# Performance work log

Hardware: AMD Instinct MI355X
Metric: run time of the kernel (lower is better)

Reference implementation:

```python
import jax, jax.numpy as jnp
import numpy as np

N, C, S = 64, 128, 12          # batch, channels, input_size
HW = S * S                      # 144
RIN = S ** 4


def setup_inputs() -> dict:
    key = jax.random.key(0)
    ks = jax.random.split(key, 6)
    x1 = jax.random.normal(ks[0], (N, C, S, S), dtype=jnp.float32)
    x2 = jax.random.normal(ks[1], (N, C, S, S), dtype=jnp.float32)
    # Linear weights stored [in, out]; scaled ~1/sqrt(fan_in) like torch default
    w1 = jax.random.normal(ks[2], (RIN, RIN // 4), dtype=jnp.float32) / np.sqrt(RIN)
    w2 = jax.random.normal(ks[3], (RIN // 4, RIN // 16), dtype=jnp.float32) / np.sqrt(RIN // 4)
    w3 = jax.random.normal(ks[4], (RIN // 16, RIN // 64), dtype=jnp.float32) / np.sqrt(RIN // 16)
    w4 = jax.random.normal(ks[5], (RIN // 64, 8), dtype=jnp.float32) / np.sqrt(RIN // 64)
    return {
        "x1": x1, "x2": x2,
        "w1": w1, "b1": jnp.zeros((RIN // 4,), jnp.float32),
        "w2": w2, "b2": jnp.zeros((RIN // 16,), jnp.float32),
        "w3": w3, "b3": jnp.zeros((RIN // 64,), jnp.float32),
        "w4": w4, "b4": jnp.zeros((8,), jnp.float32),
    }


def _l2_normalize(x):
    # torch: norm over dim=1 (channels), broadcast divide -> per-(n,h,w) unit vectors
    return x / jnp.linalg.norm(x, axis=1, keepdims=True)


def reference(x1, x2, w1, b1, w2, b2, w3, b3, w4, b4):
    n, c, h, w = x1.shape
    x1n = _l2_normalize(x1)
    x2n = _l2_normalize(x2)
    # out[n, k, i, j] = sum_c x1n[n,c,i,j] * x2n_flat[n,c,k]  (k flattens x2's HxW)
    corr = jnp.einsum('ncij,nck->nkij', x1n, x2n.reshape(n, c, h * w))  # [N, HW, H, W]
    x = corr.reshape(n, h * w * h * w)  # [N, S^4]
    x = jax.nn.relu(x @ w1 + b1)
    x = jax.nn.relu(x @ w2 + b2)
    x = jnp.tanh(x @ w3 + b3)
    H = x @ w4 + b4  # [N, 8]
    ones = jnp.ones((n, 1), dtype=H.dtype)
    return jnp.concatenate([H, ones], axis=1).reshape(n, 3, 3)
```

## Files before the change

### kernel.cpp

```cpp
#include <hip/hip_runtime.h>
#include <stdint.h>
#include <math.h>


typedef short short8 __attribute__((ext_vector_type(8)));
typedef float f32x4 __attribute__((ext_vector_type(4)));

__device__ __forceinline__ unsigned bf16u(float x) {
    return (__float_as_uint(x) + 0x8000u) >> 16;
}
__device__ __forceinline__ unsigned packbf(float a, float b) {
    return ((__float_as_uint(a) + 0x8000u) >> 16) |
           ((__float_as_uint(b) + 0x8000u) & 0xFFFF0000u);
}
__device__ __forceinline__ float bf2f(unsigned short u) {
    return __uint_as_float(((unsigned)u) << 16);
}

__global__ __launch_bounds__(1024) void kcorr2(const float* __restrict__ x1,
                                               const float* __restrict__ x2,
                                               unsigned short* __restrict__ Abuf) {
    __shared__ unsigned short s1[144 * 136];
    __shared__ unsigned short s2p[48 * 136];
    __shared__ float rn1[144], rn2p[48];
    int b = blockIdx.x;
    int n = b / 3, p = b - n * 3;
    int t = threadIdx.x;
    const float* p1 = x1 + n * 18432;
    const float* p2 = x2 + n * 18432;
#pragma unroll
    for (int i = 0; i < 18; ++i) {
        int g = t + 1024 * i;
        int c = g / 144, ij = g - c * 144;
        s1[ij * 136 + c] = (unsigned short)bf16u(p1[g]);
    }
#pragma unroll
    for (int i = 0; i < 6; ++i) {
        int g = t + 1024 * i;
        int c = g / 48, ijl = g - c * 48;
        s2p[ijl * 136 + c] = (unsigned short)bf16u(p2[c * 144 + p * 48 + ijl]);
    }
    __syncthreads();
    if (t < 144) {
        float acc = 0.f;
        for (int c = 0; c < 128; ++c) { float v = bf2f(s1[t * 136 + c]); acc += v * v; }
        rn1[t] = 1.0f / sqrtf(acc);
    } else if (t < 192) {
        int ijl = t - 144;
        float acc = 0.f;
        for (int c = 0; c < 128; ++c) { float v = bf2f(s2p[ijl * 136 + c]); acc += v * v; }
        rn2p[ijl] = 1.0f / sqrtf(acc);
    }
    __syncthreads();
    int lane = t & 63, w = t >> 6;
    int col = lane & 15, quad = lane >> 4;
    unsigned short* out = Abuf + n * 20736 + p * 48 * 144;
    for (int tt = w; tt < 27; tt += 16) {
        int ml0 = (tt / 9) * 16, n0 = (tt % 9) * 16;
        f32x4 acc = {0.f, 0.f, 0.f, 0.f};
        const short8* a0 = (const short8*)(s2p + (ml0 + col) * 136 + quad * 8);
        const short8* b0 = (const short8*)(s1 + (n0 + col) * 136 + quad * 8);
#pragma unroll
        for (int ks = 0; ks < 4; ++ks) {
            short8 a = a0[ks * 4];
            short8 bv = b0[ks * 4];
            acc = __builtin_amdgcn_mfma_f32_16x16x32_bf16(a, bv, acc, 0, 0, 0);
        }
        float rc = rn1[n0 + col];
#pragma unroll
        for (int r = 0; r < 4; ++r) {
            int rl = ml0 + quad * 4 + r;
            out[rl * 144 + n0 + col] = (unsigned short)bf16u(acc[r] * rn2p[rl] * rc);
        }
    }
}

template <int N, int KTOT, int KCHUNK>
__global__ __launch_bounds__(256) void kgemm(const unsigned short* __restrict__ A,
                                             const float* __restrict__ W,
                                             float* __restrict__ Cf) {
    int lane = threadIdx.x & 63;
    int w = threadIdx.x >> 6;
    int col = lane & 15, quad = lane >> 4;
    int c0 = blockIdx.x * 64 + w * 16;
    int kc = blockIdx.y * KCHUNK;
    const unsigned short* Ap = A + kc + quad * 8;
    const float* Wp = W + (size_t)(kc + quad * 8) * N + c0 + col;
    f32x4 acc0 = {0, 0, 0, 0}, acc1 = {0, 0, 0, 0}, acc2 = {0, 0, 0, 0}, acc3 = {0, 0, 0, 0};
#pragma unroll 2
    for (int ks = 0; ks < KCHUNK / 32; ++ks) {
        int kk = ks * 32;
        short8 a0 = *(const short8*)(Ap + (0 * 16 + col) * KTOT + kk);
        short8 a1 = *(const short8*)(Ap + (1 * 16 + col) * KTOT + kk);
        short8 a2 = *(const short8*)(Ap + (2 * 16 + col) * KTOT + kk);
        short8 a3 = *(const short8*)(Ap + (3 * 16 + col) * KTOT + kk);
        const float* wp = Wp + (size_t)kk * N;
        float b0 = wp[0 * (size_t)N];
        float b1 = wp[1 * (size_t)N];
        float b2 = wp[2 * (size_t)N];
        float b3 = wp[3 * (size_t)N];
        float b4 = wp[4 * (size_t)N];
        float b5 = wp[5 * (size_t)N];
        float b6 = wp[6 * (size_t)N];
        float b7 = wp[7 * (size_t)N];
        union { unsigned u[4]; short8 s; } bu;
        bu.u[0] = packbf(b0, b1);
        bu.u[1] = packbf(b2, b3);
        bu.u[2] = packbf(b4, b5);
        bu.u[3] = packbf(b6, b7);
        acc0 = __builtin_amdgcn_mfma_f32_16x16x32_bf16(a0, bu.s, acc0, 0, 0, 0);
        acc1 = __builtin_amdgcn_mfma_f32_16x16x32_bf16(a1, bu.s, acc1, 0, 0, 0);
        acc2 = __builtin_amdgcn_mfma_f32_16x16x32_bf16(a2, bu.s, acc2, 0, 0, 0);
        acc3 = __builtin_amdgcn_mfma_f32_16x16x32_bf16(a3, bu.s, acc3, 0, 0, 0);
    }
#pragma unroll
    for (int r = 0; r < 4; ++r) {
        int row0 = quad * 4 + r;
        atomicAdd(&Cf[(0 * 16 + row0) * N + c0 + col], acc0[r]);
        atomicAdd(&Cf[(1 * 16 + row0) * N + c0 + col], acc1[r]);
        atomicAdd(&Cf[(2 * 16 + row0) * N + c0 + col], acc2[r]);
        atomicAdd(&Cf[(3 * 16 + row0) * N + c0 + col], acc3[r]);
    }
}

template <int N, int KTOT, int KCHUNK>
__global__ __launch_bounds__(256) void kgemm2f(const float* __restrict__ Af,
                                               const float* __restrict__ bias,
                                               const float* __restrict__ W,
                                               float* __restrict__ Cf) {
    int lane = threadIdx.x & 63;
    int w = threadIdx.x >> 6;
    int col = lane & 15, quad = lane >> 4;
    int c0 = blockIdx.x * 64 + w * 16;
    if (c0 >= N) return;
    int kc = blockIdx.y * KCHUNK;
    int kb = kc + quad * 8;
    const float* Ap = Af + kb;
    const float* Wp = W + (size_t)kb * N + c0 + col;
    f32x4 acc0 = {0, 0, 0, 0}, acc1 = {0, 0, 0, 0}, acc2 = {0, 0, 0, 0}, acc3 = {0, 0, 0, 0};
#pragma unroll 2
    for (int ks = 0; ks < KCHUNK / 32; ++ks) {
        int kk = ks * 32;
        f32x4 bb0 = *(const f32x4*)(bias + kb + kk);
        f32x4 bb1 = *(const f32x4*)(bias + kb + kk + 4);
        union { unsigned u[4]; short8 s; } au[4];
#pragma unroll
        for (int i = 0; i < 4; ++i) {
            const float* ap = Ap + (size_t)(i * 16 + col) * KTOT + kk;
            f32x4 v0 = *(const f32x4*)(ap);
            f32x4 v1 = *(const f32x4*)(ap + 4);
            float r0 = fmaxf(v0[0] + bb0[0], 0.f), r1 = fmaxf(v0[1] + bb0[1], 0.f);
            float r2 = fmaxf(v0[2] + bb0[2], 0.f), r3 = fmaxf(v0[3] + bb0[3], 0.f);
            float r4 = fmaxf(v1[0] + bb1[0], 0.f), r5 = fmaxf(v1[1] + bb1[1], 0.f);
            float r6 = fmaxf(v1[2] + bb1[2], 0.f), r7 = fmaxf(v1[3] + bb1[3], 0.f);
            au[i].u[0] = packbf(r0, r1); au[i].u[1] = packbf(r2, r3);
            au[i].u[2] = packbf(r4, r5); au[i].u[3] = packbf(r6, r7);
        }
        const float* wp = Wp + (size_t)kk * N;
        float b0 = wp[0 * (size_t)N];
        float b1 = wp[1 * (size_t)N];
        float b2 = wp[2 * (size_t)N];
        float b3 = wp[3 * (size_t)N];
        float b4 = wp[4 * (size_t)N];
        float b5 = wp[5 * (size_t)N];
        float b6 = wp[6 * (size_t)N];
        float b7 = wp[7 * (size_t)N];
        union { unsigned u[4]; short8 s; } bu;
        bu.u[0] = packbf(b0, b1);
        bu.u[1] = packbf(b2, b3);
        bu.u[2] = packbf(b4, b5);
        bu.u[3] = packbf(b6, b7);
        acc0 = __builtin_amdgcn_mfma_f32_16x16x32_bf16(au[0].s, bu.s, acc0, 0, 0, 0);
        acc1 = __builtin_amdgcn_mfma_f32_16x16x32_bf16(au[1].s, bu.s, acc1, 0, 0, 0);
        acc2 = __builtin_amdgcn_mfma_f32_16x16x32_bf16(au[2].s, bu.s, acc2, 0, 0, 0);
        acc3 = __builtin_amdgcn_mfma_f32_16x16x32_bf16(au[3].s, bu.s, acc3, 0, 0, 0);
    }
#pragma unroll
    for (int r = 0; r < 4; ++r) {
        int row0 = quad * 4 + r;
        atomicAdd(&Cf[(0 * 16 + row0) * N + c0 + col], acc0[r]);
        atomicAdd(&Cf[(1 * 16 + row0) * N + c0 + col], acc1[r]);
        atomicAdd(&Cf[(2 * 16 + row0) * N + c0 + col], acc2[r]);
        atomicAdd(&Cf[(3 * 16 + row0) * N + c0 + col], acc3[r]);
    }
}

__global__ __launch_bounds__(384) void kgemm3(const float* __restrict__ C2f,
                                              const float* __restrict__ b2,
                                              const float* __restrict__ W3,
                                              float* __restrict__ C3f) {
    __shared__ float as[162];
    int n = blockIdx.x, sl = blockIdx.y;
    int t = threadIdx.x;
    int base = sl * 162;
    if (t < 162) as[t] = fmaxf(C2f[n * 1296 + base + t] + b2[base + t], 0.f);
    __syncthreads();
    if (t < 324) {
        float acc = 0.f;
        const float* wp = W3 + (size_t)base * 324 + t;
#pragma unroll 6
        for (int k = 0; k < 162; ++k) acc += as[k] * wp[k * 324];
        atomicAdd(&C3f[n * 324 + t], acc);
    }
}

__global__ __launch_bounds__(128) void kep3g4(const float* __restrict__ C3f,
                                              const float* __restrict__ b3,
                                              const float* __restrict__ W4,
                                              const float* __restrict__ b4,
                                              float* __restrict__ out) {
    __shared__ float t3[324];
    __shared__ float part[64][8];
    int n = blockIdx.x, t = threadIdx.x;
    for (int i = t; i < 324; i += 128) t3[i] = tanhf(C3f[n * 324 + i] + b3[i]);
    __syncthreads();
    if (t < 64) {
        float acc[8];
#pragma unroll
        for (int j = 0; j < 8; ++j) acc[j] = 0.f;
#pragma unroll
        for (int kk = 0; kk < 6; ++kk) {
            int k = t + 64 * kk;
            if (k < 324) {
                float v = t3[k];
                f32x4 w0 = *(const f32x4*)(W4 + k * 8);
                f32x4 w1 = *(const f32x4*)(W4 + k * 8 + 4);
                acc[0] += v * w0[0]; acc[1] += v * w0[1];
                acc[2] += v * w0[2]; acc[3] += v * w0[3];
                acc[4] += v * w1[0]; acc[5] += v * w1[1];
                acc[6] += v * w1[2]; acc[7] += v * w1[3];
            }
        }
#pragma unroll
        for (int j = 0; j < 8; ++j) part[t][j] = acc[j];
    }
    __syncthreads();
    if (t < 8) {
        float acc = b4[t];
        for (int l = 0; l < 64; ++l) acc += part[l][t];
        out[n * 9 + t] = acc;
    } else if (t == 8) {
        out[n * 9 + 8] = 1.0f;
    }
}

extern "C" void kernel_launch(void* const* d_in, const int* in_sizes, int n_in,
                              void* d_out, int out_size, void* d_ws, size_t ws_size,
                              hipStream_t stream) {
    const float* x1 = (const float*)d_in[0];
    const float* x2 = (const float*)d_in[1];
    const float* w1 = (const float*)d_in[2];
    const float* b1 = (const float*)d_in[3];
    const float* w2 = (const float*)d_in[4];
    const float* b2 = (const float*)d_in[5];
    const float* w3 = (const float*)d_in[6];
    const float* b3 = (const float*)d_in[7];
    const float* w4 = (const float*)d_in[8];
    const float* b4 = (const float*)d_in[9];
    float* out = (float*)d_out;

    char* ws = (char*)d_ws;
    unsigned short* Abuf = (unsigned short*)(ws + 0);
    float* C1f = (float*)(ws + 2654208);
    float* C2f = (float*)(ws + 3981312);
    float* C3f = (float*)(ws + 4313088);

    hipMemsetAsync(ws + 2654208, 0, 1741824, stream);
    kcorr2<<<192, 1024, 0, stream>>>(x1, x2, Abuf);
    kgemm<5184, 20736, 1152><<<dim3(81, 18), 256, 0, stream>>>(Abuf, w1, C1f);
    kgemm2f<1296, 5184, 192><<<dim3(21, 27), 256, 0, stream>>>(C1f, b1, w2, C2f);
    kgemm3<<<dim3(64, 8), 384, 0, stream>>>(C2f, b2, w3, C3f);
    kep3g4<<<64, 128, 0, stream>>>(C3f, b3, w4, b4, out);
}
```

Before: 679.6 us.

## Store activations in K-blocked [K/32][N][32] layout for coalesced MFMA operand loads

Changes the intermediate activation buffers (correlation output, C1, C2) from row-major [N][K] to a blocked layout where each 32-wide K slice holds all 64 batch rows contiguously. The GEMM A-operand loads for one k-step then read a contiguous 4 KB block instead of 64 rows strided by the full K. Producers, consumers, the atomic epilogues and the workspace offsets and memset size are all updated to match. The cost is scattered 2-byte stores in the correlation kernel and a different atomic address pattern.

```diff
diff --git a/kernel.cpp b/kernel.cpp
--- a/kernel.cpp
+++ b/kernel.cpp
@@ -54,7 +54,6 @@
     __syncthreads();
     int lane = t & 63, w = t >> 6;
     int col = lane & 15, quad = lane >> 4;
-    unsigned short* out = Abuf + n * 20736 + p * 48 * 144;
     for (int tt = w; tt < 27; tt += 16) {
         int ml0 = (tt / 9) * 16, n0 = (tt % 9) * 16;
         f32x4 acc = {0.f, 0.f, 0.f, 0.f};
@@ -70,7 +69,9 @@
 #pragma unroll
         for (int r = 0; r < 4; ++r) {
             int rl = ml0 + quad * 4 + r;
-            out[rl * 144 + n0 + col] = (unsigned short)bf16u(acc[r] * rn2p[rl] * rc);
+            int f = (p * 48 + rl) * 144 + n0 + col;
+            Abuf[(size_t)(f >> 5) * 2048 + n * 32 + (f & 31)] =
+                (unsigned short)bf16u(acc[r] * rn2p[rl] * rc);
         }
     }
 }
@@ -84,17 +85,17 @@
     int col = lane & 15, quad = lane >> 4;
     int c0 = blockIdx.x * 64 + w * 16;
     int kc = blockIdx.y * KCHUNK;
-    const unsigned short* Ap = A + kc + quad * 8;
+    const unsigned short* Ap = A + (size_t)(kc >> 5) * 2048 + quad * 8;
     const float* Wp = W + (size_t)(kc + quad * 8) * N + c0 + col;
     f32x4 acc0 = {0, 0, 0, 0}, acc1 = {0, 0, 0, 0}, acc2 = {0, 0, 0, 0}, acc3 = {0, 0, 0, 0};
 #pragma unroll 2
     for (int ks = 0; ks < KCHUNK / 32; ++ks) {
-        int kk = ks * 32;
-        short8 a0 = *(const short8*)(Ap + (0 * 16 + col) * KTOT + kk);
-        short8 a1 = *(const short8*)(Ap + (1 * 16 + col) * KTOT + kk);
-        short8 a2 = *(const short8*)(Ap + (2 * 16 + col) * KTOT + kk);
-        short8 a3 = *(const short8*)(Ap + (3 * 16 + col) * KTOT + kk);
-        const float* wp = Wp + (size_t)kk * N;
+        const unsigned short* ap = Ap + ks * 2048;
+        short8 a0 = *(const short8*)(ap + (0 * 16 + col) * 32);
+        short8 a1 = *(const short8*)(ap + (1 * 16 + col) * 32);
+        short8 a2 = *(const short8*)(ap + (2 * 16 + col) * 32);
+        short8 a3 = *(const short8*)(ap + (3 * 16 + col) * 32);
+        const float* wp = Wp + (size_t)(ks * 32) * N;
         float b0 = wp[0 * (size_t)N];
         float b1 = wp[1 * (size_t)N];
         float b2 = wp[2 * (size_t)N];
@@ -113,13 +114,15 @@
         acc2 = __builtin_amdgcn_mfma_f32_16x16x32_bf16(a2, bu.s, acc2, 0, 0, 0);
         acc3 = __builtin_amdgcn_mfma_f32_16x16x32_bf16(a3, bu.s, acc3, 0, 0, 0);
     }
+    int f = c0 + col;
+    float* cb = Cf + (size_t)(f >> 5) * 2048 + (f & 31);
 #pragma unroll
     for (int r = 0; r < 4; ++r) {
         int row0 = quad * 4 + r;
-        atomicAdd(&Cf[(0 * 16 + row0) * N + c0 + col], acc0[r]);
-        atomicAdd(&Cf[(1 * 16 + row0) * N + c0 + col], acc1[r]);
-        atomicAdd(&Cf[(2 * 16 + row0) * N + c0 + col], acc2[r]);
-        atomicAdd(&Cf[(3 * 16 + row0) * N + c0 + col], acc3[r]);
+        atomicAdd(cb + (0 * 16 + row0) * 32, acc0[r]);
+        atomicAdd(cb + (1 * 16 + row0) * 32, acc1[r]);
+        atomicAdd(cb + (2 * 16 + row0) * 32, acc2[r]);
+        atomicAdd(cb + (3 * 16 + row0) * 32, acc3[r]);
     }
 }
 
@@ -134,19 +137,18 @@
     int c0 = blockIdx.x * 64 + w * 16;
     if (c0 >= N) return;
     int kc = blockIdx.y * KCHUNK;
-    int kb = kc + quad * 8;
-    const float* Ap = Af + kb;
-    const float* Wp = W + (size_t)kb * N + c0 + col;
+    const float* Wp = W + (size_t)(kc + quad * 8) * N + c0 + col;
     f32x4 acc0 = {0, 0, 0, 0}, acc1 = {0, 0, 0, 0}, acc2 = {0, 0, 0, 0}, acc3 = {0, 0, 0, 0};
 #pragma unroll 2
     for (int ks = 0; ks < KCHUNK / 32; ++ks) {
         int kk = ks * 32;
-        f32x4 bb0 = *(const f32x4*)(bias + kb + kk);
-        f32x4 bb1 = *(const f32x4*)(bias + kb + kk + 4);
+        f32x4 bb0 = *(const f32x4*)(bias + kc + kk + quad * 8);
+        f32x4 bb1 = *(const f32x4*)(bias + kc + kk + quad * 8 + 4);
+        const float* ab = Af + (size_t)((kc + kk) >> 5) * 2048 + quad * 8;
         union { unsigned u[4]; short8 s; } au[4];
 #pragma unroll
         for (int i = 0; i < 4; ++i) {
-            const float* ap = Ap + (size_t)(i * 16 + col) * KTOT + kk;
+            const float* ap = ab + (i * 16 + col) * 32;
             f32x4 v0 = *(const f32x4*)(ap);
             f32x4 v1 = *(const f32x4*)(ap + 4);
             float r0 = fmaxf(v0[0] + bb0[0], 0.f), r1 = fmaxf(v0[1] + bb0[1], 0.f);
@@ -175,13 +177,15 @@
         acc2 = __builtin_amdgcn_mfma_f32_16x16x32_bf16(au[2].s, bu.s, acc2, 0, 0, 0);
         acc3 = __builtin_amdgcn_mfma_f32_16x16x32_bf16(au[3].s, bu.s, acc3, 0, 0, 0);
     }
+    int f = c0 + col;
+    float* cb = Cf + (size_t)(f >> 5) * 2048 + (f & 31);
 #pragma unroll
     for (int r = 0; r < 4; ++r) {
         int row0 = quad * 4 + r;
-        atomicAdd(&Cf[(0 * 16 + row0) * N + c0 + col], acc0[r]);
-        atomicAdd(&Cf[(1 * 16 + row0) * N + c0 + col], acc1[r]);
-        atomicAdd(&Cf[(2 * 16 + row0) * N + c0 + col], acc2[r]);
-        atomicAdd(&Cf[(3 * 16 + row0) * N + c0 + col], acc3[r]);
+        atomicAdd(cb + (0 * 16 + row0) * 32, acc0[r]);
+        atomicAdd(cb + (1 * 16 + row0) * 32, acc1[r]);
+        atomicAdd(cb + (2 * 16 + row0) * 32, acc2[r]);
+        atomicAdd(cb + (3 * 16 + row0) * 32, acc3[r]);
     }
 }
 
@@ -193,7 +197,11 @@
     int n = blockIdx.x, sl = blockIdx.y;
     int t = threadIdx.x;
     int base = sl * 162;
-    if (t < 162) as[t] = fmaxf(C2f[n * 1296 + base + t] + b2[base + t], 0.f);
+    if (t < 162) {
+        int k = base + t;
+        float v = C2f[(size_t)(k >> 5) * 2048 + n * 32 + (k & 31)];
+        as[t] = fmaxf(v + b2[k], 0.f);
+    }
     __syncthreads();
     if (t < 324) {
         float acc = 0.f;
@@ -263,9 +271,9 @@
     unsigned short* Abuf = (unsigned short*)(ws + 0);
     float* C1f = (float*)(ws + 2654208);
     float* C2f = (float*)(ws + 3981312);
-    float* C3f = (float*)(ws + 4313088);
-
-    hipMemsetAsync(ws + 2654208, 0, 1741824, stream);
+    float* C3f = (float*)(ws + 4317184);
+
+    hipMemsetAsync(ws + 2654208, 0, 1745920, stream);
     kcorr2<<<192, 1024, 0, stream>>>(x1, x2, Abuf);
     kgemm<5184, 20736, 1152><<<dim3(81, 18), 256, 0, stream>>>(Abuf, w1, C1f);
     kgemm2f<1296, 5184, 192><<<dim3(21, 27), 256, 0, stream>>>(C1f, b1, w2, C2f);
```

Measured after the change: 671.9 us. No clear change (-1.1%).
